# Optimization experiments

Measured on AMD Instinct MI355X. Metric: run time of the kernel, lower is better.

## Reference

```python
import jax, jax.numpy as jnp
import numpy as np

N_S, N_T, E = 50000, 50000, 600000
D_IN, D_H, D_OUT = 256, 128, 64


def setup_inputs() -> dict:
    key = jax.random.key(0)
    k1, k2, k3, k4, k5, k6 = jax.random.split(key, 6)
    edge_src = jax.random.randint(k1, (E,), 0, N_S, dtype=jnp.int32)
    edge_dst = jax.random.randint(k2, (E,), 0, N_T, dtype=jnp.int32)
    edge_index = jnp.stack([edge_src, edge_dst], axis=0)  # [2, E]
    x_s = jax.random.normal(k3, (N_S, D_IN), dtype=jnp.float32)
    x_t = jax.random.normal(k4, (N_T, D_IN), dtype=jnp.float32)
    W0 = jax.random.normal(k5, (D_IN, D_H), dtype=jnp.float32) * (1.0 / np.sqrt(D_IN))
    W1 = jax.random.normal(k6, (D_H, D_OUT), dtype=jnp.float32) * (1.0 / np.sqrt(D_H))
    return {"edge_index": edge_index, "x_s": x_s, "x_t": x_t, "W0": W0, "W1": W1}


def gcn_conv(x, src, dst, W):
    """PyG GCNConv, bias=False: D^{-1/2}(A+I)D^{-1/2} (x @ W)."""
    N = x.shape[0]
    h = x @ W  # [N, out]
    loops = jnp.arange(N, dtype=src.dtype)
    s = jnp.concatenate([src, loops])  # add self-loops
    d = jnp.concatenate([dst, loops])
    deg = jax.ops.segment_sum(jnp.ones_like(d, dtype=h.dtype), d, num_segments=N)
    dinv = jnp.where(deg > 0, jax.lax.rsqrt(deg), 0.0)
    norm = dinv[s] * dinv[d]  # [E+N]
    return jax.ops.segment_sum(h[s] * norm[:, None], d, num_segments=N)


def reference(edge_index, x_s, x_t, W0, W1):
    n_s = x_s.shape[0]
    src = edge_index[0]
    dst = edge_index[1] + n_s  # targets live in the x_t block
    acts = [jax.nn.relu, lambda v: v]
    Ws = [W0, W1]
    for W, act in zip(Ws, acts):
        x = jnp.concatenate([x_s, x_t], axis=0)
        x = act(gcn_conv(x, src, dst, W))
        x_s, x_t = x[:n_s], x[n_s:]
    return (x_s, x_t)
```

## Files before the change

kernel.cpp:

```cpp
#include <hip/hip_runtime.h>
#include <cstdint>
#include <cstddef>

typedef unsigned short u16;
typedef unsigned int   u32;
typedef __attribute__((ext_vector_type(8))) short bf16x8;
typedef __attribute__((ext_vector_type(4))) float f32x4;

#define D_IN  256
#define D_H   128
#define D_OUT 64

__device__ __forceinline__ float bf2f(u16 u){
  union { u32 i; float f; } v; v.i = ((u32)u) << 16; return v.f;
}
__device__ __forceinline__ u16 f2bf(float f){
  union { float f; u32 i; } v; v.f = f;
  u32 r = (v.i + 0x7fffu + ((v.i >> 16) & 1u)) >> 16;
  return (u16)r;
}

__global__ void k_wprep(const float* __restrict__ W0, const float* __restrict__ W1,
                        u16* __restrict__ W0t, u16* __restrict__ W1t,
                        int* __restrict__ deg, int n_t){
  int i = blockIdx.x * 256 + threadIdx.x;
  if (i < 128 * 256){
    int n = i >> 8, k = i & 255;
    W0t[i] = f2bf(W0[(size_t)k * 128 + n]);
  } else if (i < 128 * 256 + 64 * 128){
    int j = i - 128 * 256;
    int n = j >> 7, k = j & 127;
    W1t[j] = f2bf(W1[(size_t)k * 64 + n]);
  } else if (i - (128 * 256 + 64 * 128) < n_t){
    deg[i - (128 * 256 + 64 * 128)] = 0;
  }
}

__global__ void k_deg(const int* __restrict__ dst, int E, int* __restrict__ deg){
  int e = blockIdx.x * 256 + threadIdx.x;
  if (e < E) atomicAdd(&deg[dst[e]], 1);
}

__global__ __launch_bounds__(256) void k_bsum(const int* __restrict__ deg, int N,
                                              int* __restrict__ bsum){
  __shared__ int s[256];
  int tid = threadIdx.x;
  int i = blockIdx.x * 256 + tid;
  s[tid] = (i < N) ? deg[i] : 0;
  __syncthreads();
  for (int o = 128; o > 0; o >>= 1){
    if (tid < o) s[tid] += s[tid + o];
    __syncthreads();
  }
  if (tid == 0) bsum[blockIdx.x] = s[0];
}

__global__ __launch_bounds__(256) void k_off(const int* __restrict__ deg, int N,
                                             const int* __restrict__ bsum, int nb,
                                             int* __restrict__ off, int* __restrict__ cursor,
                                             float* __restrict__ dinv){
  __shared__ int s[256];
  __shared__ int sbase[256];
  const int tid = threadIdx.x;
  const int bid = blockIdx.x;
  const int i   = bid * 256 + tid;
  int acc = 0;
  for (int j = tid; j < bid; j += 256) acc += bsum[j];
  sbase[tid] = acc;
  int v = (i < N) ? deg[i] : 0;
  s[tid] = v;
  __syncthreads();
  for (int o = 128; o > 0; o >>= 1){
    if (tid < o) sbase[tid] += sbase[tid + o];
    __syncthreads();
  }
  for (int o = 1; o < 256; o <<= 1){
    int t = (tid >= o) ? s[tid - o] : 0;
    __syncthreads();
    s[tid] += t;
    __syncthreads();
  }
  if (i < N){
    int excl = s[tid] - v + sbase[0];
    off[i] = excl;
    cursor[i] = excl;
    dinv[i] = rsqrtf((float)v + 1.0f);
  }
}

__global__ void k_fill(const int* __restrict__ src, const int* __restrict__ dst,
                       int E, int* __restrict__ cursor, int* __restrict__ csr){
  int e = blockIdx.x * 256 + threadIdx.x;
  if (e < E){
    int d = dst[e];
    int p = atomicAdd(&cursor[d], 1);
    csr[p] = src[e];
  }
}

__global__ __launch_bounds__(256) void k_gemm1(
    const float* __restrict__ Xs, const float* __restrict__ Xt,
    const u16* __restrict__ W0t, int M, int n_s,
    u16* __restrict__ out)
{
  __shared__ u16 As[64 * 256];
  const int t    = threadIdx.x;
  const int wave = t >> 6, lane = t & 63;
  const int lm   = lane & 15, quad = lane >> 4;
  const int row0 = blockIdx.x * 64;

  {
    float4 st[16];
    #pragma unroll
    for (int i = 0; i < 16; i++){
      int r = row0 + wave + i * 4;
      const float* p;
      if (r < n_s)    p = Xs + (size_t)r * D_IN + lane * 4;
      else if (r < M) p = Xt + (size_t)(r - n_s) * D_IN + lane * 4;
      else            p = Xs + lane * 4;
      st[i] = *(const float4*)p;
    }
    #pragma unroll
    for (int i = 0; i < 16; i++){
      int r = wave + i * 4;
      u16 tmp[4];
      tmp[0] = f2bf(st[i].x); tmp[1] = f2bf(st[i].y);
      tmp[2] = f2bf(st[i].z); tmp[3] = f2bf(st[i].w);
      int c = (lane * 4) ^ ((r & 7) << 3);
      *(int2*)&As[r * 256 + c] = *(const int2*)tmp;
    }
  }
  __syncthreads();

  f32x4 acc[8];
  const f32x4 z = {0.f, 0.f, 0.f, 0.f};
  #pragma unroll
  for (int nf = 0; nf < 8; nf++) acc[nf] = z;

  const u16* pb = W0t + (size_t)lm * D_IN + quad * 8;
  int4 b[2][8];
  #pragma unroll
  for (int nf = 0; nf < 8; nf++)
    b[0][nf] = *(const int4*)(pb + (size_t)nf * 16 * D_IN);

  const int ra  = wave * 16 + lm;
  const int rsw = (ra & 7) << 3;
  const u16* arow = As + ra * 256;

  #pragma unroll
  for (int kk = 0; kk < 8; kk++){
    const int cur = kk & 1, nxt = cur ^ 1;
    if (kk < 7){
      const int ko = (kk + 1) * 32;
      #pragma unroll
      for (int nf = 0; nf < 8; nf++)
        b[nxt][nf] = *(const int4*)(pb + (size_t)nf * 16 * D_IN + ko);
    }
    bf16x8 af = *(const bf16x8*)(arow + ((kk * 32 + quad * 8) ^ rsw));
    #pragma unroll
    for (int nf = 0; nf < 8; nf++)
      acc[nf] = __builtin_amdgcn_mfma_f32_16x16x32_bf16(
          af, *(const bf16x8*)&b[cur][nf], acc[nf], 0, 0, 0);
  }

  {
    int rbase = row0 + wave * 16 + quad * 4;
    #pragma unroll
    for (int rr = 0; rr < 4; rr++){
      int m = rbase + rr;
      if (m >= M) continue;
      u16* op = out + (size_t)m * D_H + lm;
      #pragma unroll
      for (int nf = 0; nf < 8; nf++)
        op[nf * 16] = f2bf(acc[nf][rr]);
    }
  }
}

__global__ __launch_bounds__(256) void k_aggf(
    const int* __restrict__ off, const int* __restrict__ deg,
    const int* __restrict__ csr, const float* __restrict__ dinv,
    u16* __restrict__ h1, int n_s, int n_t)
{
  int w    = (blockIdx.x * 256 + threadIdx.x) >> 6;
  int lane = threadIdx.x & 63;
  if (w >= n_t) return;
  const int g = lane >> 4;
  const int c = lane & 15;
  int start = off[w];
  int n     = deg[w];

  float r[8], p[8];
  #pragma unroll
  for (int q = 0; q < 8; q++){ r[q] = 0.f; p[q] = 0.f; }

  int i = 0;
  for (; i + 8 <= n; i += 8){
    int sa = csr[start + i + g];
    int sb = csr[start + i + 4 + g];
    int4 da = *(const int4*)(h1 + (size_t)sa * D_H + c * 8);
    int4 db = *(const int4*)(h1 + (size_t)sb * D_H + c * 8);
    const u16* ha = (const u16*)&da;
    const u16* hb = (const u16*)&db;
    #pragma unroll
    for (int q = 0; q < 8; q++){
      float va = bf2f(ha[q]), vb = bf2f(hb[q]);
      r[q] += va + vb;
      p[q] += fmaxf(va, 0.f) + fmaxf(vb, 0.f);
    }
  }
  for (; i < n; i += 4){
    if (i + g < n){
      int sa = csr[start + i + g];
      int4 da = *(const int4*)(h1 + (size_t)sa * D_H + c * 8);
      const u16* ha = (const u16*)&da;
      #pragma unroll
      for (int q = 0; q < 8; q++){
        float va = bf2f(ha[q]);
        r[q] += va;
        p[q] += fmaxf(va, 0.f);
      }
    }
  }

  #pragma unroll
  for (int q = 0; q < 8; q++){
    r[q] += __shfl_xor(r[q], 16, 64);
    r[q] += __shfl_xor(r[q], 32, 64);
    p[q] += __shfl_xor(p[q], 16, 64);
    p[q] += __shfl_xor(p[q], 32, 64);
  }

  if (g == 0){
    float di  = dinv[w];
    float di2 = di * di;
    u16* selfp = h1 + (size_t)(n_s + w) * D_H + c * 8;
    int4 hs = *(const int4*)selfp;
    const u16* hh = (const u16*)&hs;
    u16 ob[8];
    #pragma unroll
    for (int q = 0; q < 8; q++){
      float zq = fmaxf(di * r[q] + di2 * bf2f(hh[q]), 0.f);
      float uq = di * p[q] + di2 * zq;
      ob[q] = f2bf(uq);
    }
    *(int4*)selfp = *(int4*)ob;
  }
}

__device__ __forceinline__ bf16x8 relu_bf(int4 v, bool relu){
  const u16* s = (const u16*)&v;
  u16 tmp[8];
  #pragma unroll
  for (int q = 0; q < 8; q++){
    u16 x = s[q];
    tmp[q] = (relu && (x & 0x8000u)) ? (u16)0 : x;
  }
  return *(const bf16x8*)tmp;
}

__global__ __launch_bounds__(256) void k_gemm2(
    const u16* __restrict__ h1, const u16* __restrict__ W1t,
    int M, int n_s, float* __restrict__ out)
{
  const int t    = threadIdx.x;
  const int wave = t >> 6, lane = t & 63;
  const int lm   = lane & 15, quad = lane >> 4;
  const int rowW = blockIdx.x * 128 + wave * 32;

  int r0 = rowW + lm, r1 = rowW + 16 + lm;
  const bool relu0 = (r0 < n_s), relu1 = (r1 < n_s);
  int c0 = (r0 < M) ? r0 : 0, c1 = (r1 < M) ? r1 : 0;
  const u16* pa0 = h1 + (size_t)c0 * D_H + quad * 8;
  const u16* pa1 = h1 + (size_t)c1 * D_H + quad * 8;
  const u16* pb  = W1t + (size_t)lm * D_H + quad * 8;

  f32x4 acc[2][4];
  const f32x4 z = {0.f, 0.f, 0.f, 0.f};
  #pragma unroll
  for (int i = 0; i < 2; i++)
    #pragma unroll
    for (int j = 0; j < 4; j++) acc[i][j] = z;

  int4 a[2][2], b[2][4];
  a[0][0] = *(const int4*)(pa0);
  a[0][1] = *(const int4*)(pa1);
  #pragma unroll
  for (int nf = 0; nf < 4; nf++)
    b[0][nf] = *(const int4*)(pb + (size_t)nf * 16 * D_H);

  #pragma unroll
  for (int kk = 0; kk < 4; kk++){
    const int cur = kk & 1, nxt = cur ^ 1;
    if (kk < 3){
      const int ko = (kk + 1) * 32;
      a[nxt][0] = *(const int4*)(pa0 + ko);
      a[nxt][1] = *(const int4*)(pa1 + ko);
      #pragma unroll
      for (int nf = 0; nf < 4; nf++)
        b[nxt][nf] = *(const int4*)(pb + (size_t)nf * 16 * D_H + ko);
    }
    bf16x8 af[2];
    af[0] = relu_bf(a[cur][0], relu0);
    af[1] = relu_bf(a[cur][1], relu1);
    #pragma unroll
    for (int mi = 0; mi < 2; mi++)
      #pragma unroll
      for (int nf = 0; nf < 4; nf++)
        acc[mi][nf] = __builtin_amdgcn_mfma_f32_16x16x32_bf16(
            af[mi], *(const bf16x8*)&b[cur][nf], acc[mi][nf], 0, 0, 0);
  }

  #pragma unroll
  for (int mi = 0; mi < 2; mi++){
    int rbase = rowW + mi * 16 + quad * 4;
    #pragma unroll
    for (int rr = 0; rr < 4; rr++){
      int m = rbase + rr;
      if (m >= M) continue;
      float* op = out + (size_t)m * D_OUT + lm;
      #pragma unroll
      for (int nf = 0; nf < 4; nf++)
        op[nf * 16] = acc[mi][nf][rr];
    }
  }
}

static inline size_t alup(size_t x){ return (x + 255) & ~(size_t)255; }

extern "C" void kernel_launch(void* const* d_in, const int* in_sizes, int n_in,
                              void* d_out, int out_size, void* d_ws, size_t ws_size,
                              hipStream_t stream)
{
  const int*   ei = (const int*)d_in[0];
  const float* xs = (const float*)d_in[1];
  const float* xt = (const float*)d_in[2];
  const float* W0 = (const float*)d_in[3];
  const float* W1 = (const float*)d_in[4];
  const int E   = in_sizes[0] / 2;
  const int n_s = in_sizes[1] / D_IN;
  const int n_t = in_sizes[2] / D_IN;
  const int M   = n_s + n_t;
  const int* src = ei;
  const int* dst = ei + E;
  const int nb_t = (n_t + 255) / 256;

  char* p = (char*)d_ws;
  int*   deg    = (int*)p;    p += alup((size_t)n_t * 4);
  int*   off    = (int*)p;    p += alup((size_t)n_t * 4);
  int*   cursor = (int*)p;    p += alup((size_t)n_t * 4);
  float* dinv   = (float*)p;  p += alup((size_t)n_t * 4);
  int*   bsum   = (int*)p;    p += alup((size_t)nb_t * 4);
  int*   csr    = (int*)p;    p += alup((size_t)E * 4);
  u16*   W0t    = (u16*)p;    p += alup((size_t)D_H * D_IN * 2);
  u16*   W1t    = (u16*)p;    p += alup((size_t)D_OUT * D_H * 2);
  u16*   h1     = (u16*)p;    p += alup((size_t)M * D_H * 2);

  const int wprep_n = 128*256 + 64*128 + n_t;
  k_wprep <<<(wprep_n + 255) / 256, 256, 0, stream>>>(W0, W1, W0t, W1t, deg, n_t);
  k_deg   <<<(E + 255) / 256, 256, 0, stream>>>(dst, E, deg);
  k_bsum  <<<nb_t, 256, 0, stream>>>(deg, n_t, bsum);
  k_off   <<<nb_t, 256, 0, stream>>>(deg, n_t, bsum, nb_t, off, cursor, dinv);
  k_fill  <<<(E + 255) / 256, 256, 0, stream>>>(src, dst, E, cursor, csr);

  k_gemm1<<<(M + 63) / 64, 256, 0, stream>>>(xs, xt, W0t, M, n_s, h1);
  k_aggf <<<(n_t + 3) / 4, 256, 0, stream>>>(off, deg, csr, dinv, h1, n_s, n_t);
  k_gemm2<<<(M + 127) / 128, 256, 0, stream>>>(h1, W1t, M, n_s, (float*)d_out);
}
```

Measured before the change: 292.1 us.

## Stage weights in LDS and stream activations directly to registers in both GEMMs

Both GEMM kernels now load the weight matrix once per block into swizzled shared memory. Activation rows are read straight from global memory into registers with a two-deep prefetch, and converted to bf16 on the fly. Before, gemm1 staged activations in LDS and every wave read its weights from global memory. Blocks grow to 512 threads (8 waves, 16 rows each), so the weights are reused across more rows. In exchange each block pays a weight fill into LDS (64KB for gemm1), which may limit occupancy.

```diff
diff --git a/kernel.cpp b/kernel.cpp
--- a/kernel.cpp
+++ b/kernel.cpp
@@ -98,36 +98,38 @@
   }
 }
 
-__global__ __launch_bounds__(256) void k_gemm1(
+__global__ __launch_bounds__(512, 3) void k_gemm1(
     const float* __restrict__ Xs, const float* __restrict__ Xt,
     const u16* __restrict__ W0t, int M, int n_s,
     u16* __restrict__ out)
 {
-  __shared__ u16 As[64 * 256];
+  __shared__ u16 Bs[128 * 256];
   const int t    = threadIdx.x;
   const int wave = t >> 6, lane = t & 63;
   const int lm   = lane & 15, quad = lane >> 4;
-  const int row0 = blockIdx.x * 64;
+  const int gw   = blockIdx.x * 8 + wave;
+  const int row  = gw * 16 + lm;
+
+  int cr = (row < M) ? row : 0;
+  const float* pa = ((cr < n_s) ? (Xs + (size_t)cr * D_IN)
+                                : (Xt + (size_t)(cr - n_s) * D_IN)) + quad * 8;
+
+  float4 a[2][2];
+  a[0][0] = *(const float4*)(pa + 0);
+  a[0][1] = *(const float4*)(pa + 4);
+  a[1][0] = *(const float4*)(pa + 32);
+  a[1][1] = *(const float4*)(pa + 36);
 
   {
-    float4 st[16];
-    #pragma unroll
-    for (int i = 0; i < 16; i++){
-      int r = row0 + wave + i * 4;
-      const float* p;
-      if (r < n_s)    p = Xs + (size_t)r * D_IN + lane * 4;
-      else if (r < M) p = Xt + (size_t)(r - n_s) * D_IN + lane * 4;
-      else            p = Xs + lane * 4;
-      st[i] = *(const float4*)p;
-    }
-    #pragma unroll
-    for (int i = 0; i < 16; i++){
-      int r = wave + i * 4;
-      u16 tmp[4];
-      tmp[0] = f2bf(st[i].x); tmp[1] = f2bf(st[i].y);
-      tmp[2] = f2bf(st[i].z); tmp[3] = f2bf(st[i].w);
-      int c = (lane * 4) ^ ((r & 7) << 3);
-      *(int2*)&As[r * 256 + c] = *(const int2*)tmp;
+    const int n = t >> 2;
+    const int c = t & 3;
+    const u16* wsrc = W0t + (size_t)n * 256 + c * 64;
+    char* brow = (char*)Bs + n * 512;
+    const int sw = (n & 15) << 4;
+    #pragma unroll
+    for (int j = 0; j < 8; j++){
+      int off = (c * 128 + j * 16) ^ sw;
+      *(int4*)(brow + off) = *(const int4*)(wsrc + j * 8);
     }
   }
   __syncthreads();
@@ -137,34 +139,34 @@
   #pragma unroll
   for (int nf = 0; nf < 8; nf++) acc[nf] = z;
 
-  const u16* pb = W0t + (size_t)lm * D_IN + quad * 8;
-  int4 b[2][8];
-  #pragma unroll
-  for (int nf = 0; nf < 8; nf++)
-    b[0][nf] = *(const int4*)(pb + (size_t)nf * 16 * D_IN);
-
-  const int ra  = wave * 16 + lm;
-  const int rsw = (ra & 7) << 3;
-  const u16* arow = As + ra * 256;
+  const char* bb = (const char*)Bs + lm * 512;
+  const int lmx = lm << 4;
 
   #pragma unroll
   for (int kk = 0; kk < 8; kk++){
-    const int cur = kk & 1, nxt = cur ^ 1;
-    if (kk < 7){
-      const int ko = (kk + 1) * 32;
+    const int cur = kk & 1;
+    bf16x8 af;
+    {
+      const float* fa = (const float*)&a[cur][0];
+      u16 tmp[8];
       #pragma unroll
-      for (int nf = 0; nf < 8; nf++)
-        b[nxt][nf] = *(const int4*)(pb + (size_t)nf * 16 * D_IN + ko);
-    }
-    bf16x8 af = *(const bf16x8*)(arow + ((kk * 32 + quad * 8) ^ rsw));
-    #pragma unroll
-    for (int nf = 0; nf < 8; nf++)
-      acc[nf] = __builtin_amdgcn_mfma_f32_16x16x32_bf16(
-          af, *(const bf16x8*)&b[cur][nf], acc[nf], 0, 0, 0);
+      for (int q = 0; q < 8; q++) tmp[q] = f2bf(fa[q]);
+      af = *(const bf16x8*)tmp;
+    }
+    if (kk < 6){
+      a[cur][0] = *(const float4*)(pa + (kk + 2) * 32);
+      a[cur][1] = *(const float4*)(pa + (kk + 2) * 32 + 4);
+    }
+    const int koff = (kk * 64 + quad * 16) ^ lmx;
+    #pragma unroll
+    for (int nf = 0; nf < 8; nf++){
+      bf16x8 bf = *(const bf16x8*)(bb + nf * 8192 + koff);
+      acc[nf] = __builtin_amdgcn_mfma_f32_16x16x32_bf16(af, bf, acc[nf], 0, 0, 0);
+    }
   }
 
   {
-    int rbase = row0 + wave * 16 + quad * 4;
+    int rbase = gw * 16 + quad * 4;
     #pragma unroll
     for (int rr = 0; rr < 4; rr++){
       int m = rbase + rr;
@@ -259,61 +261,63 @@
   return *(const bf16x8*)tmp;
 }
 
-__global__ __launch_bounds__(256) void k_gemm2(
+__global__ __launch_bounds__(512, 3) void k_gemm2(
     const u16* __restrict__ h1, const u16* __restrict__ W1t,
     int M, int n_s, float* __restrict__ out)
 {
+  __shared__ u16 Bs[64 * 128];
   const int t    = threadIdx.x;
   const int wave = t >> 6, lane = t & 63;
   const int lm   = lane & 15, quad = lane >> 4;
-  const int rowW = blockIdx.x * 128 + wave * 32;
-
-  int r0 = rowW + lm, r1 = rowW + 16 + lm;
-  const bool relu0 = (r0 < n_s), relu1 = (r1 < n_s);
-  int c0 = (r0 < M) ? r0 : 0, c1 = (r1 < M) ? r1 : 0;
-  const u16* pa0 = h1 + (size_t)c0 * D_H + quad * 8;
-  const u16* pa1 = h1 + (size_t)c1 * D_H + quad * 8;
-  const u16* pb  = W1t + (size_t)lm * D_H + quad * 8;
-
-  f32x4 acc[2][4];
+  const int gw   = blockIdx.x * 8 + wave;
+  const int row  = gw * 16 + lm;
+
+  int cr = (row < M) ? row : 0;
+  const bool relu = (row < n_s);
+  const u16* pa = h1 + (size_t)cr * D_H + quad * 8;
+
+  int4 a[2];
+  a[0] = *(const int4*)(pa);
+  a[1] = *(const int4*)(pa + 32);
+
+  {
+    const int n = t >> 3;
+    const int c = t & 7;
+    const u16* wsrc = W1t + (size_t)n * 128 + c * 16;
+    char* brow = (char*)Bs + n * 256;
+    const int sw = (n & 15) << 4;
+    #pragma unroll
+    for (int j = 0; j < 2; j++){
+      int off = (c * 32 + j * 16) ^ sw;
+      *(int4*)(brow + off) = *(const int4*)(wsrc + j * 8);
+    }
+  }
+  __syncthreads();
+
+  f32x4 acc[4];
   const f32x4 z = {0.f, 0.f, 0.f, 0.f};
   #pragma unroll
-  for (int i = 0; i < 2; i++)
-    #pragma unroll
-    for (int j = 0; j < 4; j++) acc[i][j] = z;
-
-  int4 a[2][2], b[2][4];
-  a[0][0] = *(const int4*)(pa0);
-  a[0][1] = *(const int4*)(pa1);
-  #pragma unroll
-  for (int nf = 0; nf < 4; nf++)
-    b[0][nf] = *(const int4*)(pb + (size_t)nf * 16 * D_H);
+  for (int nf = 0; nf < 4; nf++) acc[nf] = z;
+
+  const char* bb = (const char*)Bs + lm * 256;
+  const int lmx = lm << 4;
 
   #pragma unroll
   for (int kk = 0; kk < 4; kk++){
-    const int cur = kk & 1, nxt = cur ^ 1;
-    if (kk < 3){
-      const int ko = (kk + 1) * 32;
-      a[nxt][0] = *(const int4*)(pa0 + ko);
-      a[nxt][1] = *(const int4*)(pa1 + ko);
-      #pragma unroll
-      for (int nf = 0; nf < 4; nf++)
-        b[nxt][nf] = *(const int4*)(pb + (size_t)nf * 16 * D_H + ko);
-    }
-    bf16x8 af[2];
-    af[0] = relu_bf(a[cur][0], relu0);
-    af[1] = relu_bf(a[cur][1], relu1);
-    #pragma unroll
-    for (int mi = 0; mi < 2; mi++)
-      #pragma unroll
-      for (int nf = 0; nf < 4; nf++)
-        acc[mi][nf] = __builtin_amdgcn_mfma_f32_16x16x32_bf16(
-            af[mi], *(const bf16x8*)&b[cur][nf], acc[mi][nf], 0, 0, 0);
-  }
-
-  #pragma unroll
-  for (int mi = 0; mi < 2; mi++){
-    int rbase = rowW + mi * 16 + quad * 4;
+    const int cur = kk & 1;
+    bf16x8 af = relu_bf(a[cur], relu);
+    if (kk < 2)
+      a[cur] = *(const int4*)(pa + (kk + 2) * 32);
+    const int koff = (kk * 64 + quad * 16) ^ lmx;
+    #pragma unroll
+    for (int nf = 0; nf < 4; nf++){
+      bf16x8 bf = *(const bf16x8*)(bb + nf * 4096 + koff);
+      acc[nf] = __builtin_amdgcn_mfma_f32_16x16x32_bf16(af, bf, acc[nf], 0, 0, 0);
+    }
+  }
+
+  {
+    int rbase = gw * 16 + quad * 4;
     #pragma unroll
     for (int rr = 0; rr < 4; rr++){
       int m = rbase + rr;
@@ -321,7 +325,7 @@
       float* op = out + (size_t)m * D_OUT + lm;
       #pragma unroll
       for (int nf = 0; nf < 4; nf++)
-        op[nf * 16] = acc[mi][nf][rr];
+        op[nf * 16] = acc[nf][rr];
     }
   }
 }
@@ -363,7 +367,7 @@
   k_off   <<<nb_t, 256, 0, stream>>>(deg, n_t, bsum, nb_t, off, cursor, dinv);
   k_fill  <<<(E + 255) / 256, 256, 0, stream>>>(src, dst, E, cursor, csr);
 
-  k_gemm1<<<(M + 63) / 64, 256, 0, stream>>>(xs, xt, W0t, M, n_s, h1);
+  k_gemm1<<<(M + 127) / 128, 512, 0, stream>>>(xs, xt, W0t, M, n_s, h1);
   k_aggf <<<(n_t + 3) / 4, 256, 0, stream>>>(off, deg, csr, dinv, h1, n_s, n_t);
-  k_gemm2<<<(M + 127) / 128, 256, 0, stream>>>(h1, W1t, M, n_s, (float*)d_out);
-}
+  k_gemm2<<<(M + 127) / 128, 512, 0, stream>>>(h1, W1t, M, n_s, (float*)d_out);
+}
```

Measured after the change: 260.8 us. 1.12x faster.
